# Kernel optimization log

Hardware: AMD Instinct MI355X
Metric: run time of the kernel (lower is better)

Reference implementation:

```python
import jax, jax.numpy as jnp
import numpy as np

H = 1024
V = 128000


def setup_inputs() -> dict:
    key = jax.random.key(0)
    ks = jax.random.split(key, 9)
    s = 0.02  # param init scale for numerical sanity
    return {
        "input_ids": jax.random.randint(ks[0], (1,), 0, V),
        "hidden": jax.random.normal(ks[1], (1, 1, H), dtype=jnp.float32),
        "emb": jax.random.normal(ks[2], (V, H), dtype=jnp.float32) * s,
        "W_ih": jax.random.normal(ks[3], (3 * H, H), dtype=jnp.float32) * s,
        "W_hh": jax.random.normal(ks[4], (3 * H, H), dtype=jnp.float32) * s,
        "b_ih": jax.random.normal(ks[5], (3 * H,), dtype=jnp.float32) * s,
        "b_hh": jax.random.normal(ks[6], (3 * H,), dtype=jnp.float32) * s,
        "W_out": jax.random.normal(ks[7], (V, H), dtype=jnp.float32) * s,
        "b_out": jax.random.normal(ks[8], (V,), dtype=jnp.float32) * s,
    }


def reference(input_ids, hidden, emb, W_ih, W_hh, b_ih, b_hh, W_out, b_out):
    # embedding lookup for the single token, then ReLU (matches F.relu on embed)
    x = jax.nn.relu(emb[input_ids[0]])            # (H,)
    h0 = hidden[0, 0]                             # (H,)
    # PyTorch GRU cell: gates ordered [r, z, n]
    gi = W_ih @ x + b_ih                          # (3H,)
    gh = W_hh @ h0 + b_hh                         # (3H,)
    r = jax.nn.sigmoid(gi[:H] + gh[:H])
    z = jax.nn.sigmoid(gi[H:2 * H] + gh[H:2 * H])
    n = jnp.tanh(gi[2 * H:] + r * gh[2 * H:])
    h1 = (1.0 - z) * n + z * h0                   # (H,)
    # output projection + log-softmax over vocab (dim=1 on (1, V))
    logits = W_out @ h1 + b_out                   # (V,)
    logp = jax.nn.log_softmax(logits)[None, :]    # (1, V)
    return logp, h1[None, None, :]                # ((1,V), (1,1,H))
```

## Files before the change

kernel.cpp:

```cpp
#include <hip/hip_runtime.h>
#include <math.h>

#define H 1024
#define V 128000
#define G3H 3072
#define NWL 16000

#define WS_GI   0
#define WS_GH   G3H
#define WS_PART 8192

typedef float f32x4 __attribute__((ext_vector_type(4)));

#define DOT4(w_, x_) fmaf((w_).x,(x_).x, fmaf((w_).y,(x_).y, fmaf((w_).z,(x_).z, (w_).w*(x_).w)))

__global__ __launch_bounds__(256) void gates_matvec(
    const int* __restrict__ ids, const float* __restrict__ hidden,
    const float* __restrict__ emb,
    const float* __restrict__ W_ih, const float* __restrict__ W_hh,
    const float* __restrict__ b_ih, const float* __restrict__ b_hh,
    float* __restrict__ ws) {
  const int tid  = threadIdx.x;
  const int lane = tid & 63;
  const int wid  = blockIdx.x * 4 + (tid >> 6);
  const bool isGi = (wid < 1536);
  const int row0 = (isGi ? wid : wid - 1536) * 2;

  const float* Wm = isGi ? W_ih : W_hh;
  const float* xp = isGi ? (emb + (size_t)ids[0] * H) : hidden;

  f32x4 x0 = ((const f32x4*)xp)[lane];
  f32x4 x1 = ((const f32x4*)xp)[lane + 64];
  f32x4 x2 = ((const f32x4*)xp)[lane + 128];
  f32x4 x3 = ((const f32x4*)xp)[lane + 192];
  if (isGi) {
    x0.x=fmaxf(x0.x,0.f); x0.y=fmaxf(x0.y,0.f); x0.z=fmaxf(x0.z,0.f); x0.w=fmaxf(x0.w,0.f);
    x1.x=fmaxf(x1.x,0.f); x1.y=fmaxf(x1.y,0.f); x1.z=fmaxf(x1.z,0.f); x1.w=fmaxf(x1.w,0.f);
    x2.x=fmaxf(x2.x,0.f); x2.y=fmaxf(x2.y,0.f); x2.z=fmaxf(x2.z,0.f); x2.w=fmaxf(x2.w,0.f);
    x3.x=fmaxf(x3.x,0.f); x3.y=fmaxf(x3.y,0.f); x3.z=fmaxf(x3.z,0.f); x3.w=fmaxf(x3.w,0.f);
  }

  const f32x4* wa = (const f32x4*)(Wm + (size_t)row0 * H);
  const f32x4* wb = (const f32x4*)(Wm + (size_t)(row0 + 1) * H);
  const f32x4 a0 = __builtin_nontemporal_load(wa + lane);
  const f32x4 a1 = __builtin_nontemporal_load(wa + lane + 64);
  const f32x4 a2 = __builtin_nontemporal_load(wa + lane + 128);
  const f32x4 a3 = __builtin_nontemporal_load(wa + lane + 192);
  const f32x4 b0 = __builtin_nontemporal_load(wb + lane);
  const f32x4 b1 = __builtin_nontemporal_load(wb + lane + 64);
  const f32x4 b2 = __builtin_nontemporal_load(wb + lane + 128);
  const f32x4 b3 = __builtin_nontemporal_load(wb + lane + 192);
  float pa = (DOT4(a0,x0) + DOT4(a1,x1)) + (DOT4(a2,x2) + DOT4(a3,x3));
  float pb = (DOT4(b0,x0) + DOT4(b1,x1)) + (DOT4(b2,x2) + DOT4(b3,x3));
#pragma unroll
  for (int off = 1; off < 64; off <<= 1) {
    pa += __shfl_xor(pa, off);
    pb += __shfl_xor(pb, off);
  }
  if (lane < 2) {
    const int row = row0 + lane;
    const float s = (lane == 0) ? pa : pb;
    if (isGi) ws[WS_GI + row] = s + b_ih[row];
    else      ws[WS_GH + row] = s + b_hh[row];
  }
}

__global__ __launch_bounds__(256) void logits_lse(
    const float* __restrict__ hidden, const float* __restrict__ ws_in,
    const float* __restrict__ W_out, const float* __restrict__ b_out,
    float* __restrict__ d_out, float* __restrict__ ws_part) {
  __shared__ __align__(16) float h1s[H];
  const int tid = threadIdx.x;

  for (int i = tid; i < H; i += 256) {
    const float r = 1.f / (1.f + expf(-(ws_in[WS_GI + i]     + ws_in[WS_GH + i])));
    const float z = 1.f / (1.f + expf(-(ws_in[WS_GI + H + i] + ws_in[WS_GH + H + i])));
    const float n = tanhf(ws_in[WS_GI + 2*H + i] + r * ws_in[WS_GH + 2*H + i]);
    h1s[i] = (1.f - z) * n + z * hidden[i];
  }
  __syncthreads();
  if (blockIdx.x == 0) {
    for (int i = tid; i < H; i += 256) d_out[V + i] = h1s[i];
  }

  const int lane = tid & 63;
  const int wid  = blockIdx.x * 4 + (tid >> 6);
  const int row0 = wid * 8;

  const f32x4 x0 = ((const f32x4*)h1s)[lane];
  const f32x4 x1 = ((const f32x4*)h1s)[lane + 64];
  const f32x4 x2 = ((const f32x4*)h1s)[lane + 128];
  const f32x4 x3 = ((const f32x4*)h1s)[lane + 192];

  float p[8];
#pragma unroll
  for (int pr = 0; pr < 4; ++pr) {
    const f32x4* wa = (const f32x4*)(W_out + (size_t)(row0 + 2*pr)     * H);
    const f32x4* wb = (const f32x4*)(W_out + (size_t)(row0 + 2*pr + 1) * H);
    const f32x4 a0 = __builtin_nontemporal_load(wa + lane);
    const f32x4 a1 = __builtin_nontemporal_load(wa + lane + 64);
    const f32x4 a2 = __builtin_nontemporal_load(wa + lane + 128);
    const f32x4 a3 = __builtin_nontemporal_load(wa + lane + 192);
    const f32x4 b0 = __builtin_nontemporal_load(wb + lane);
    const f32x4 b1 = __builtin_nontemporal_load(wb + lane + 64);
    const f32x4 b2 = __builtin_nontemporal_load(wb + lane + 128);
    const f32x4 b3 = __builtin_nontemporal_load(wb + lane + 192);
    p[2*pr]   = (DOT4(a0,x0) + DOT4(a1,x1)) + (DOT4(a2,x2) + DOT4(a3,x3));
    p[2*pr+1] = (DOT4(b0,x0) + DOT4(b1,x1)) + (DOT4(b2,x2) + DOT4(b3,x3));
  }

#pragma unroll
  for (int off = 1; off < 64; off <<= 1) {
#pragma unroll
    for (int r = 0; r < 8; ++r) p[r] += __shfl_xor(p[r], off);
  }

  const float4 bo0 = ((const float4*)(b_out + row0))[0];
  const float4 bo1 = ((const float4*)(b_out + row0))[1];
  const float l0 = p[0] + bo0.x, l1 = p[1] + bo0.y, l2 = p[2] + bo0.z, l3 = p[3] + bo0.w;
  const float l4 = p[4] + bo1.x, l5 = p[5] + bo1.y, l6 = p[6] + bo1.z, l7 = p[7] + bo1.w;

  if (lane == 0) d_out[row0 + 0] = l0;
  if (lane == 1) d_out[row0 + 1] = l1;
  if (lane == 2) d_out[row0 + 2] = l2;
  if (lane == 3) d_out[row0 + 3] = l3;
  if (lane == 4) d_out[row0 + 4] = l4;
  if (lane == 5) d_out[row0 + 5] = l5;
  if (lane == 6) d_out[row0 + 6] = l6;
  if (lane == 7) d_out[row0 + 7] = l7;

  const float m = fmaxf(fmaxf(fmaxf(l0,l1), fmaxf(l2,l3)), fmaxf(fmaxf(l4,l5), fmaxf(l6,l7)));
  const float S = expf(l0-m) + expf(l1-m) + expf(l2-m) + expf(l3-m)
                + expf(l4-m) + expf(l5-m) + expf(l6-m) + expf(l7-m);
  if (lane == 0) {
    ws_part[2*wid]     = m;
    ws_part[2*wid + 1] = S;
  }
}

__global__ __launch_bounds__(256) void lse_norm(
    float* __restrict__ d_out, const float* __restrict__ ws_part) {
  __shared__ float redm[256], reds[256];
  const int tid = threadIdx.x;

  float m = -INFINITY, S = 0.f;
  for (int b = tid; b < NWL; b += 256) {
    const float mb = ws_part[2*b], sb = ws_part[2*b+1];
    const float mn = fmaxf(m, mb);
    S = S * expf(m - mn) + sb * expf(mb - mn);
    m = mn;
  }
  redm[tid] = m; reds[tid] = S;
  __syncthreads();
  for (int s = 128; s > 0; s >>= 1) {
    if (tid < s) {
      const float m2 = redm[tid + s], s2 = reds[tid + s];
      const float mn = fmaxf(redm[tid], m2);
      reds[tid] = reds[tid] * expf(redm[tid] - mn) + s2 * expf(m2 - mn);
      redm[tid] = mn;
    }
    __syncthreads();
  }
  const float lse = redm[0] + logf(reds[0]);

  const int i = blockIdx.x * 256 + tid;
  d_out[i] -= lse;
}

extern "C" void kernel_launch(void* const* d_in, const int* in_sizes, int n_in,
                              void* d_out, int out_size, void* d_ws, size_t ws_size,
                              hipStream_t stream) {
  const int*   ids    = (const int*)d_in[0];
  const float* hidden = (const float*)d_in[1];
  const float* emb    = (const float*)d_in[2];
  const float* W_ih   = (const float*)d_in[3];
  const float* W_hh   = (const float*)d_in[4];
  const float* b_ih   = (const float*)d_in[5];
  const float* b_hh   = (const float*)d_in[6];
  const float* W_out  = (const float*)d_in[7];
  const float* b_out  = (const float*)d_in[8];
  float* out = (float*)d_out;
  float* ws  = (float*)d_ws;

  gates_matvec<<<768, 256, 0, stream>>>(ids, hidden, emb, W_ih, W_hh, b_ih, b_hh, ws);
  logits_lse<<<4000, 256, 0, stream>>>(hidden, ws, W_out, b_out, out, ws + WS_PART);
  lse_norm<<<500, 256, 0, stream>>>(out, ws + WS_PART);
}
```

Measured before the change: 115.8 us.

## Use persistent grid-stride waves with online softmax stats in logits kernel

The logits kernel now launches 1024 blocks instead of 4000, and each wave loops over groups of four rows in grid-stride order. It keeps a running max and sum-exp across its groups instead of covering one fixed set of eight rows. This removes the per-block recomputation of the GRU hidden state (about 4000 blocks each evaluating sigmoid and tanh for 1024 elements) and shrinks the partial-stats array that the normalisation kernel scans. The trade-off is fewer bytes in flight per iteration, since each iteration loads four rows rather than eight, and a serial dependency chain in the loop.

```diff
diff --git a/kernel.cpp b/kernel.cpp
--- a/kernel.cpp
+++ b/kernel.cpp
@@ -4,7 +4,10 @@
 #define H 1024
 #define V 128000
 #define G3H 3072
-#define NWL 16000
+
+#define K2_BLOCKS 1024
+#define K2_WAVES  (K2_BLOCKS * 4)
+#define K2_GROUPS (V / 4)
 
 #define WS_GI   0
 #define WS_GH   G3H
@@ -65,7 +68,7 @@
   }
 }
 
-__global__ __launch_bounds__(256) void logits_lse(
+__global__ __launch_bounds__(256, 4) void logits_lse(
     const float* __restrict__ hidden, const float* __restrict__ ws_in,
     const float* __restrict__ W_out, const float* __restrict__ b_out,
     float* __restrict__ d_out, float* __restrict__ ws_part) {
@@ -85,53 +88,62 @@
 
   const int lane = tid & 63;
   const int wid  = blockIdx.x * 4 + (tid >> 6);
-  const int row0 = wid * 8;
 
   const f32x4 x0 = ((const f32x4*)h1s)[lane];
   const f32x4 x1 = ((const f32x4*)h1s)[lane + 64];
   const f32x4 x2 = ((const f32x4*)h1s)[lane + 128];
   const f32x4 x3 = ((const f32x4*)h1s)[lane + 192];
 
-  float p[8];
+  float m = -INFINITY, S = 0.f;
+
+#pragma unroll 1
+  for (int g = wid; g < K2_GROUPS; g += K2_WAVES) {
+    const int row0 = g * 4;
+    const f32x4* w = (const f32x4*)(W_out + (size_t)row0 * H);
+
+    const f32x4 a0 = __builtin_nontemporal_load(w + lane);
+    const f32x4 a1 = __builtin_nontemporal_load(w + lane + 64);
+    const f32x4 a2 = __builtin_nontemporal_load(w + lane + 128);
+    const f32x4 a3 = __builtin_nontemporal_load(w + lane + 192);
+    const f32x4 b0 = __builtin_nontemporal_load(w + lane + 256);
+    const f32x4 b1 = __builtin_nontemporal_load(w + lane + 320);
+    const f32x4 b2 = __builtin_nontemporal_load(w + lane + 384);
+    const f32x4 b3 = __builtin_nontemporal_load(w + lane + 448);
+    const f32x4 c0 = __builtin_nontemporal_load(w + lane + 512);
+    const f32x4 c1 = __builtin_nontemporal_load(w + lane + 576);
+    const f32x4 c2 = __builtin_nontemporal_load(w + lane + 640);
+    const f32x4 c3 = __builtin_nontemporal_load(w + lane + 704);
+    const f32x4 d0 = __builtin_nontemporal_load(w + lane + 768);
+    const f32x4 d1 = __builtin_nontemporal_load(w + lane + 832);
+    const f32x4 d2 = __builtin_nontemporal_load(w + lane + 896);
+    const f32x4 d3 = __builtin_nontemporal_load(w + lane + 960);
+
+    float p0 = (DOT4(a0,x0) + DOT4(a1,x1)) + (DOT4(a2,x2) + DOT4(a3,x3));
+    float p1 = (DOT4(b0,x0) + DOT4(b1,x1)) + (DOT4(b2,x2) + DOT4(b3,x3));
+    float p2 = (DOT4(c0,x0) + DOT4(c1,x1)) + (DOT4(c2,x2) + DOT4(c3,x3));
+    float p3 = (DOT4(d0,x0) + DOT4(d1,x1)) + (DOT4(d2,x2) + DOT4(d3,x3));
+
 #pragma unroll
-  for (int pr = 0; pr < 4; ++pr) {
-    const f32x4* wa = (const f32x4*)(W_out + (size_t)(row0 + 2*pr)     * H);
-    const f32x4* wb = (const f32x4*)(W_out + (size_t)(row0 + 2*pr + 1) * H);
-    const f32x4 a0 = __builtin_nontemporal_load(wa + lane);
-    const f32x4 a1 = __builtin_nontemporal_load(wa + lane + 64);
-    const f32x4 a2 = __builtin_nontemporal_load(wa + lane + 128);
-    const f32x4 a3 = __builtin_nontemporal_load(wa + lane + 192);
-    const f32x4 b0 = __builtin_nontemporal_load(wb + lane);
-    const f32x4 b1 = __builtin_nontemporal_load(wb + lane + 64);
-    const f32x4 b2 = __builtin_nontemporal_load(wb + lane + 128);
-    const f32x4 b3 = __builtin_nontemporal_load(wb + lane + 192);
-    p[2*pr]   = (DOT4(a0,x0) + DOT4(a1,x1)) + (DOT4(a2,x2) + DOT4(a3,x3));
-    p[2*pr+1] = (DOT4(b0,x0) + DOT4(b1,x1)) + (DOT4(b2,x2) + DOT4(b3,x3));
-  }
-
-#pragma unroll
-  for (int off = 1; off < 64; off <<= 1) {
-#pragma unroll
-    for (int r = 0; r < 8; ++r) p[r] += __shfl_xor(p[r], off);
-  }
-
-  const float4 bo0 = ((const float4*)(b_out + row0))[0];
-  const float4 bo1 = ((const float4*)(b_out + row0))[1];
-  const float l0 = p[0] + bo0.x, l1 = p[1] + bo0.y, l2 = p[2] + bo0.z, l3 = p[3] + bo0.w;
-  const float l4 = p[4] + bo1.x, l5 = p[5] + bo1.y, l6 = p[6] + bo1.z, l7 = p[7] + bo1.w;
-
-  if (lane == 0) d_out[row0 + 0] = l0;
-  if (lane == 1) d_out[row0 + 1] = l1;
-  if (lane == 2) d_out[row0 + 2] = l2;
-  if (lane == 3) d_out[row0 + 3] = l3;
-  if (lane == 4) d_out[row0 + 4] = l4;
-  if (lane == 5) d_out[row0 + 5] = l5;
-  if (lane == 6) d_out[row0 + 6] = l6;
-  if (lane == 7) d_out[row0 + 7] = l7;
-
-  const float m = fmaxf(fmaxf(fmaxf(l0,l1), fmaxf(l2,l3)), fmaxf(fmaxf(l4,l5), fmaxf(l6,l7)));
-  const float S = expf(l0-m) + expf(l1-m) + expf(l2-m) + expf(l3-m)
-                + expf(l4-m) + expf(l5-m) + expf(l6-m) + expf(l7-m);
+    for (int off = 1; off < 64; off <<= 1) {
+      p0 += __shfl_xor(p0, off);
+      p1 += __shfl_xor(p1, off);
+      p2 += __shfl_xor(p2, off);
+      p3 += __shfl_xor(p3, off);
+    }
+
+    const float4 bo = *(const float4*)(b_out + row0);
+    const float l0 = p0 + bo.x, l1 = p1 + bo.y, l2 = p2 + bo.z, l3 = p3 + bo.w;
+
+    const float sel = (lane == 0) ? l0 : (lane == 1) ? l1 : (lane == 2) ? l2 : l3;
+    if (lane < 4) d_out[row0 + lane] = sel;
+
+    const float m4 = fmaxf(fmaxf(l0, l1), fmaxf(l2, l3));
+    const float mn = fmaxf(m, m4);
+    S = S * expf(m - mn)
+      + expf(l0 - mn) + expf(l1 - mn) + expf(l2 - mn) + expf(l3 - mn);
+    m = mn;
+  }
+
   if (lane == 0) {
     ws_part[2*wid]     = m;
     ws_part[2*wid + 1] = S;
@@ -144,7 +156,7 @@
   const int tid = threadIdx.x;
 
   float m = -INFINITY, S = 0.f;
-  for (int b = tid; b < NWL; b += 256) {
+  for (int b = tid; b < K2_WAVES; b += 256) {
     const float mb = ws_part[2*b], sb = ws_part[2*b+1];
     const float mn = fmaxf(m, mb);
     S = S * expf(m - mn) + sb * expf(mb - mn);
@@ -183,6 +195,6 @@
   float* ws  = (float*)d_ws;
 
   gates_matvec<<<768, 256, 0, stream>>>(ids, hidden, emb, W_ih, W_hh, b_ih, b_hh, ws);
-  logits_lse<<<4000, 256, 0, stream>>>(hidden, ws, W_out, b_out, out, ws + WS_PART);
+  logits_lse<<<K2_BLOCKS, 256, 0, stream>>>(hidden, ws, W_out, b_out, out, ws + WS_PART);
   lse_norm<<<500, 256, 0, stream>>>(out, ws + WS_PART);
 }
```

New measurement: 102.7 us. 1.13x faster.
